# Kernel tuning notes

Measured on AMD Instinct MI355X. Metric: run time of the kernel, lower is better.

## Reference

```python
import jax, jax.numpy as jnp
import numpy as np

HIDDEN, HEADS, HDIM = 1024, 8, 64
B, S = 4, 8192
LN_EPS = 1e-6


def setup_inputs() -> dict:
    key = jax.random.key(0)
    ks = jax.random.split(key, 12)
    inner = HEADS * HDIM
    sd = HIDDEN ** -0.5
    return {
        "x": jax.random.normal(ks[0], (B, S, HIDDEN), jnp.float32),
        "Wq": jax.random.normal(ks[1], (HIDDEN, inner), jnp.float32) * sd,
        "bq": jnp.zeros((inner,), jnp.float32),
        "Wk": jax.random.normal(ks[2], (HIDDEN, inner), jnp.float32) * sd,
        "bk": jnp.zeros((inner,), jnp.float32),
        "Wv": jax.random.normal(ks[3], (HIDDEN, inner), jnp.float32) * sd,
        "bv": jnp.zeros((inner,), jnp.float32),
        "Wo": jax.random.normal(ks[4], (inner, HIDDEN), jnp.float32) * (inner ** -0.5),
        "bo": jnp.zeros((HIDDEN,), jnp.float32),
        "alpha": jnp.ones((HEADS, HDIM), jnp.float32),
        "aug_param": jax.random.normal(ks[5], (1, HEADS, HDIM), jnp.float32),
        "ln_scale": jnp.ones((HIDDEN,), jnp.float32),
        "ln_bias": jnp.zeros((HIDDEN,), jnp.float32),
    }


def reference(x, Wq, bq, Wk, bk, Wv, bv, Wo, bo, alpha, aug_param, ln_scale, ln_bias):
    b, s, _ = x.shape
    h, d = alpha.shape
    scale = d ** -0.5
    q = (x @ Wq + bq).reshape(b, s, h, d)
    k = (x @ Wk + bk).reshape(b, s, h, d)
    v = (x @ Wv + bv).reshape(b, s, h, d)
    decay = jax.nn.sigmoid(alpha)  # (h, d)

    def step(state, qkv):
        q_t, k_t, v_t = qkv  # each (b, h, d)
        attn = jax.nn.softmax(jnp.einsum('bhd,bhd->bh', q_t, k_t) * scale, axis=-1)
        new_state = decay * state + (1.0 - decay) * attn[..., None] * v_t
        return new_state, new_state

    qs = jnp.moveaxis(q, 1, 0)  # (s, b, h, d)
    ks_ = jnp.moveaxis(k, 1, 0)
    vs = jnp.moveaxis(v, 1, 0)
    init = jnp.zeros((b, h, d), x.dtype)
    _, states = jax.lax.scan(step, init, (qs, ks_, vs))
    states = jnp.moveaxis(states, 0, 1)  # (b, s, h, d)

    aug = jax.nn.sigmoid(q * aug_param)  # aug_param (1,h,d) broadcasts over (b,s,h,d)
    out = (q * states + aug).reshape(b, s, h * d)
    out = out @ Wo + bo
    mean = jnp.mean(out, axis=-1, keepdims=True)
    var = jnp.var(out, axis=-1, keepdims=True)
    return (out - mean) * jax.lax.rsqrt(var + LN_EPS) * ln_scale + ln_bias
```

## Files before the change

kernel.cpp:

```cpp
#include <hip/hip_runtime.h>
#include <hip/hip_bf16.h>


#define HIDDEN 1024
#define HEADS 8
#define HDIM 64
#define INNER 512
#define BATCH 4
#define SEQ 8192
#define ROWS (BATCH*SEQ)
#define NCHUNK 128
#define CHLEN 64

typedef unsigned short u16;
typedef unsigned int u32;
typedef __attribute__((ext_vector_type(8))) short bf16x8;
typedef __attribute__((ext_vector_type(4))) float f32x4;

__device__ __forceinline__ float b2f(u16 u) { return __uint_as_float(((u32)u) << 16); }
__device__ __forceinline__ u16 f2b(float f) {
  u32 u = __float_as_uint(f);
  u32 r = u + 0x7fffu + ((u >> 16) & 1u);
  return (u16)(r >> 16);
}
__device__ __forceinline__ u32 pack2(float a, float b) {
  return (u32)f2b(a) | ((u32)f2b(b) << 16);
}

#define GLOAD_LDS16(gp, lp)                                                  \
  __builtin_amdgcn_global_load_lds(                                          \
      (const __attribute__((address_space(1))) u32*)(gp),                    \
      (__attribute__((address_space(3))) u32*)(lp), 16, 0, 0)

__global__ __launch_bounds__(256) void prep_x(const float* __restrict__ x,
                                              u16* __restrict__ xb) {
  size_t i = ((size_t)blockIdx.x * 256 + threadIdx.x) * 8;
  float4 a = *(const float4*)(x + i);
  float4 b = *(const float4*)(x + i + 4);
  uint4 w = {pack2(a.x, a.y), pack2(a.z, a.w), pack2(b.x, b.y), pack2(b.z, b.w)};
  *(uint4*)(xb + i) = w;
}

__global__ __launch_bounds__(256) void prep_w(
    const float* __restrict__ Wq, const float* __restrict__ Wk,
    const float* __restrict__ Wv, const float* __restrict__ Wo,
    const float* __restrict__ bq, const float* __restrict__ bk,
    const float* __restrict__ bv,
    u16* __restrict__ Wt, u16* __restrict__ Wot, float* __restrict__ bcat) {
  const int WELEM = HIDDEN * INNER;
  int idx = blockIdx.x * 256 + threadIdx.x;
  if (idx < 3 * WELEM) {
    int z = idx / WELEM;
    int rem = idx - z * WELEM;
    int n = rem >> 10;
    int k = rem & 1023;
    const float* W = (z == 0) ? Wq : (z == 1) ? Wk : Wv;
    Wt[idx] = f2b(W[k * INNER + n]);
  } else {
    int rem = idx - 3 * WELEM;
    int n = rem >> 9;
    int k = rem & 511;
    Wot[rem] = f2b(Wo[k * HIDDEN + n]);
  }
  if (idx < 3 * INNER) {
    int z = idx >> 9;
    int n = idx & 511;
    bcat[idx] = (z == 0) ? bq[n] : (z == 1) ? bk[n] : bv[n];
  }
}

template <int K, bool SPLIT3>
__global__ __launch_bounds__(512, 2) void gemm_8ph(
    const u16* __restrict__ A, const u16* __restrict__ Bt,
    const float* __restrict__ bias,
    void* __restrict__ out0, void* __restrict__ out1, void* __restrict__ out2,
    int nTilesN) {
  constexpr int NT = K / 32;
  __shared__ u16 lds[4][16384];

  const int nwg = gridDim.x;
  const int chunk = nwg >> 3;
  const int bid = blockIdx.x;
  const int lin = (bid & 7) * chunk + (bid >> 3);
  const int nt = lin % nTilesN;
  const int mt = lin / nTilesN;
  const int m0 = mt * 256, n0 = nt * 256;
  const int N = nTilesN * 256;

  const int tid = threadIdx.x;
  const int lane = tid & 63;
  const int w = tid >> 6;
  const int wm = w >> 2;
  const int wn = w & 3;
  const int r16 = lane & 15, kq = lane >> 4;

  const int rt = tid >> 2;
  const int cg = (((tid & 3) << 3)) ^ (((rt >> 1) & 3) << 3);
  const u16* Ag = A + (size_t)(m0 + rt) * K + cg;
  const u16* Bg = Bt + (size_t)(n0 + rt) * K + cg;
  const int ldst = w * 512;

#define STAGE_AB(slot, kt)                                                    \
  {                                                                           \
    GLOAD_LDS16(Ag + (size_t)(kt) * 32, &lds[slot][ldst]);                    \
    GLOAD_LDS16(Ag + (size_t)(kt) * 32 + (size_t)128 * K,                     \
                &lds[slot][4096 + ldst]);                                     \
    GLOAD_LDS16(Bg + (size_t)(kt) * 32, &lds[slot][8192 + ldst]);             \
    GLOAD_LDS16(Bg + (size_t)(kt) * 32 + (size_t)128 * K,                     \
                &lds[slot][12288 + ldst]);                                    \
  }

  const int xk = (kq << 3) ^ (((r16 >> 1) & 3) << 3);
  const int aO = (wm * 128 + r16) * 32 + xk;
  const int bO = 8192 + (wn * 64 + r16) * 32 + xk;

  f32x4 acc[8][4] = {};

#define TILE(t_, STG, VMW)                                                     \
  {                                                                            \
    STG;                                                                       \
    const u16* sl = &lds[(t_) & 3][0];                                         \
    bf16x8 af0[4], af1[4], bfv4[4];                                            \
    _Pragma("unroll") for (int i = 0; i < 4; i++)                              \
        af0[i] = *(const bf16x8*)&sl[aO + i * 512];                            \
    _Pragma("unroll") for (int j = 0; j < 4; j++)                              \
        bfv4[j] = *(const bf16x8*)&sl[bO + j * 512];                           \
    __builtin_amdgcn_sched_barrier(0);                                         \
    _Pragma("unroll") for (int i = 0; i < 4; i++)                              \
        af1[i] = *(const bf16x8*)&sl[aO + (i + 4) * 512];                      \
    __builtin_amdgcn_sched_barrier(0);                                         \
    __builtin_amdgcn_s_setprio(1);                                             \
    _Pragma("unroll") for (int i = 0; i < 4; i++)                              \
        _Pragma("unroll") for (int j = 0; j < 4; j++)                          \
            acc[i][j] =                                                        \
        __builtin_amdgcn_mfma_f32_16x16x32_bf16(af0[i], bfv4[j], acc[i][j], 0, 0, 0); \
    __builtin_amdgcn_s_setprio(0);                                             \
    __builtin_amdgcn_sched_barrier(0);                                         \
    __builtin_amdgcn_s_setprio(1);                                             \
    _Pragma("unroll") for (int i = 0; i < 4; i++)                              \
        _Pragma("unroll") for (int j = 0; j < 4; j++)                          \
            acc[i + 4][j] =                                                    \
        __builtin_amdgcn_mfma_f32_16x16x32_bf16(af1[i], bfv4[j], acc[i + 4][j], 0, 0, 0); \
    __builtin_amdgcn_s_setprio(0);                                             \
    VMW;                                                                       \
    __builtin_amdgcn_sched_barrier(0);                                         \
    __builtin_amdgcn_s_barrier();                                              \
  }

#define VM8 asm volatile("s_waitcnt vmcnt(8)" ::: "memory")
#define VM4 asm volatile("s_waitcnt vmcnt(4)" ::: "memory")
#define VM0 asm volatile("s_waitcnt vmcnt(0)" ::: "memory")
#define NOSTG ((void)0)
#define NOVM ((void)0)

  STAGE_AB(0, 0);
  STAGE_AB(1, 1);
  STAGE_AB(2, 2);
  VM8;
  __builtin_amdgcn_sched_barrier(0);
  __builtin_amdgcn_s_barrier();

  for (int t = 0; t < NT - 3; ++t) {
    TILE(t, STAGE_AB((t + 3) & 3, t + 3), VM8);
  }
  TILE(NT - 3, NOSTG, VM4);
  TILE(NT - 2, NOSTG, VM0);
  TILE(NT - 1, NOSTG, NOVM);
#undef TILE
#undef STAGE_AB
#undef VM8
#undef VM4
#undef VM0
#undef NOSTG
#undef NOVM

  float* fl = (float*)(&lds[0][0]) + w * 4096;
  const int zsel = SPLIT3 ? ((n0 + wn * 64) >> 9) : 0;
  u16* ob = SPLIT3 ? (u16*)((zsel == 0) ? out0 : (zsel == 1) ? out1 : out2)
                   : (u16*)out0;
  const int OC = SPLIT3 ? INNER : N;
  const int colloc = (lane & 7) * 8;
  const int gcol = (SPLIT3 ? ((n0 + wn * 64) & 511) : (n0 + wn * 64)) + colloc;
  const int lrowr = lane >> 3;
  float bvj[4];
#pragma unroll
  for (int j = 0; j < 4; j++) bvj[j] = bias[n0 + wn * 64 + j * 16 + r16];

#pragma unroll
  for (int pass = 0; pass < 4; ++pass) {
#pragma unroll
    for (int ii = 0; ii < 2; ++ii) {
#pragma unroll
      for (int j = 0; j < 4; ++j) {
#pragma unroll
        for (int q = 0; q < 4; ++q)
          fl[(ii * 16 + kq * 4 + q) * 68 + j * 16 + r16] =
              acc[pass * 2 + ii][j][q] + bvj[j];
      }
    }
#pragma unroll
    for (int inst = 0; inst < 4; ++inst) {
      int lr = inst * 8 + lrowr;
      float4 f0 = *(float4*)&fl[lr * 68 + colloc];
      float4 f1 = *(float4*)&fl[lr * 68 + colloc + 4];
      uint4 wv = {pack2(f0.x, f0.y), pack2(f0.z, f0.w),
                  pack2(f1.x, f1.y), pack2(f1.z, f1.w)};
      size_t grow = (size_t)(m0 + wm * 128 + pass * 32 + lr);
      *(uint4*)&ob[grow * OC + gcol] = wv;
    }
  }
}

template <bool A_BF16>
__global__ __launch_bounds__(256) void gemm128(
    const void* __restrict__ Aany, const u16* __restrict__ BtBase,
    const float* __restrict__ bias0, const float* __restrict__ bias1,
    const float* __restrict__ bias2,
    void* __restrict__ out0, void* __restrict__ out1, void* __restrict__ out2,
    int K) {
  __shared__ u16 As[128 * 32];
  __shared__ u16 Bs[128 * 32];
  const int N = gridDim.x * 128;
  const int z = blockIdx.z;
  const u16* Bt = BtBase + (size_t)z * N * K;
  const float* bias = (z == 0) ? bias0 : (z == 1) ? bias1 : bias2;
  void* Out = (z == 0) ? out0 : (z == 1) ? out1 : out2;
  const int tid = threadIdx.x;
  const int m0 = blockIdx.y * 128;
  const int n0 = blockIdx.x * 128;
  const int lane = tid & 63;
  const int wid = tid >> 6;
  const int wm = wid >> 1, wn = wid & 1;
  const int r16 = lane & 15, kq = lane >> 4;
  const int r = tid >> 1;
  const int half = tid & 1;
  f32x4 acc[4][4] = {};
  for (int k0 = 0; k0 < K; k0 += 32) {
    __syncthreads();
    if (A_BF16) {
      const u16* Ab = (const u16*)Aany;
      const int4* src = (const int4*)(Ab + (size_t)(m0 + r) * K + k0 + half * 16);
      int4 v0 = src[0];
      int4 v1 = src[1];
      *(int4*)&As[r * 32 + half * 16] = v0;
      *(int4*)&As[r * 32 + half * 16 + 8] = v1;
    } else {
      const float* Af = (const float*)Aany;
      const float4* src = (const float4*)(Af + (size_t)(m0 + r) * K + k0 + half * 16);
      float4 f0 = src[0], f1 = src[1], f2 = src[2], f3 = src[3];
      uint4 w0 = {pack2(f0.x, f0.y), pack2(f0.z, f0.w), pack2(f1.x, f1.y), pack2(f1.z, f1.w)};
      uint4 w1 = {pack2(f2.x, f2.y), pack2(f2.z, f2.w), pack2(f3.x, f3.y), pack2(f3.z, f3.w)};
      *(uint4*)&As[r * 32 + half * 16] = w0;
      *(uint4*)&As[r * 32 + half * 16 + 8] = w1;
    }
    {
      const int4* src = (const int4*)(Bt + (size_t)(n0 + r) * K + k0 + half * 16);
      int4 v0 = src[0];
      int4 v1 = src[1];
      *(int4*)&Bs[r * 32 + half * 16] = v0;
      *(int4*)&Bs[r * 32 + half * 16 + 8] = v1;
    }
    __syncthreads();
    bf16x8 a[4], b[4];
#pragma unroll
    for (int i = 0; i < 4; i++)
      a[i] = *(const bf16x8*)&As[(wm * 64 + i * 16 + r16) * 32 + kq * 8];
#pragma unroll
    for (int j = 0; j < 4; j++)
      b[j] = *(const bf16x8*)&Bs[(wn * 64 + j * 16 + r16) * 32 + kq * 8];
#pragma unroll
    for (int i = 0; i < 4; i++)
#pragma unroll
      for (int j = 0; j < 4; j++)
        acc[i][j] = __builtin_amdgcn_mfma_f32_16x16x32_bf16(a[i], b[j], acc[i][j], 0, 0, 0);
  }
#pragma unroll
  for (int j = 0; j < 4; j++) {
    int col = n0 + wn * 64 + j * 16 + r16;
    float bv = bias[col];
#pragma unroll
    for (int i = 0; i < 4; i++) {
#pragma unroll
      for (int q = 0; q < 4; q++) {
        int row = m0 + wm * 64 + i * 16 + kq * 4 + q;
        float v = acc[i][j][q] + bv;
        ((u16*)Out)[(size_t)row * N + col] = f2b(v);
      }
    }
  }
}

__global__ __launch_bounds__(256) void attn_kernel(
    const u16* __restrict__ qb, const u16* __restrict__ kb,
    float* __restrict__ attn) {
  int lane = threadIdx.x & 63;
  int wid = threadIdx.x >> 6;
  size_t t = (size_t)blockIdx.x * 4 + wid;
  int4 qv = *(const int4*)(qb + t * INNER + lane * 8);
  int4 kv = *(const int4*)(kb + t * INNER + lane * 8);
  const u16* qu = (const u16*)&qv;
  const u16* ku = (const u16*)&kv;
  float s = 0.f;
#pragma unroll
  for (int j = 0; j < 8; j++) s += b2f(qu[j]) * b2f(ku[j]);
  s += __shfl_xor(s, 1);
  s += __shfl_xor(s, 2);
  s += __shfl_xor(s, 4);
  s *= 0.125f;
  float mx = s;
  mx = fmaxf(mx, __shfl_xor(mx, 8));
  mx = fmaxf(mx, __shfl_xor(mx, 16));
  mx = fmaxf(mx, __shfl_xor(mx, 32));
  float e = __expf(s - mx);
  float sm = e;
  sm += __shfl_xor(sm, 8);
  sm += __shfl_xor(sm, 16);
  sm += __shfl_xor(sm, 32);
  float a = e / sm;
  if ((lane & 7) == 0) attn[t * HEADS + (lane >> 3)] = a;
}

__global__ __launch_bounds__(512) void scan_phase1(
    const u16* __restrict__ vb, const float* __restrict__ attn,
    const float* __restrict__ alpha, float* __restrict__ ends) {
  int hd = threadIdx.x;
  int h = hd >> 6;
  int c = blockIdx.x, b = blockIdx.y;
  float decay = 1.f / (1.f + __expf(-alpha[hd]));
  float om = 1.f - decay;
  size_t base = (size_t)b * SEQ + (size_t)c * CHLEN;
  float st = 0.f;
#pragma unroll 8
  for (int i = 0; i < CHLEN; i++) {
    size_t t = base + i;
    float a = attn[t * HEADS + h];
    float v = b2f(vb[t * INNER + hd]);
    st = decay * st + om * a * v;
  }
  ends[((size_t)b * NCHUNK + c) * INNER + hd] = st;
}

__global__ __launch_bounds__(512) void scan_phase2(
    const float* __restrict__ ends, const float* __restrict__ alpha,
    float* __restrict__ carries) {
  int hd = threadIdx.x;
  int b = blockIdx.x;
  float decay = 1.f / (1.f + __expf(-alpha[hd]));
  float dL = __powf(decay, (float)CHLEN);
  float carry = 0.f;
#pragma unroll 8
  for (int c = 0; c < NCHUNK; c++) {
    size_t idx = ((size_t)b * NCHUNK + c) * INNER + hd;
    carries[idx] = carry;
    carry = dL * carry + ends[idx];
  }
}

__global__ __launch_bounds__(512) void scan_phase3(
    const u16* __restrict__ qb, const u16* __restrict__ vb,
    const float* __restrict__ attn, const float* __restrict__ alpha,
    const float* __restrict__ augp, const float* __restrict__ carries,
    u16* __restrict__ outpre) {
  int hd = threadIdx.x;
  int h = hd >> 6;
  int c = blockIdx.x, b = blockIdx.y;
  float decay = 1.f / (1.f + __expf(-alpha[hd]));
  float om = 1.f - decay;
  float ap = augp[hd];
  float st = carries[((size_t)b * NCHUNK + c) * INNER + hd];
  size_t base = (size_t)b * SEQ + (size_t)c * CHLEN;
#pragma unroll 4
  for (int i = 0; i < CHLEN; i++) {
    size_t t = base + i;
    float a = attn[t * HEADS + h];
    float v = b2f(vb[t * INNER + hd]);
    st = decay * st + om * a * v;
    float q = b2f(qb[t * INNER + hd]);
    float aug = 1.f / (1.f + __expf(-q * ap));
    outpre[t * INNER + hd] = f2b(q * st + aug);
  }
}

__global__ __launch_bounds__(256) void ln_kernel(
    const u16* __restrict__ outln, float* __restrict__ out,
    const float* __restrict__ lns, const float* __restrict__ lnb) {
  size_t row = blockIdx.x;
  int tid = threadIdx.x;
  uint2 rv = *(const uint2*)(outln + row * HIDDEN + tid * 4);
  const u16* p = (const u16*)&rv;
  float v0 = b2f(p[0]), v1 = b2f(p[1]), v2 = b2f(p[2]), v3 = b2f(p[3]);
  float s = v0 + v1 + v2 + v3;
  float ss = v0 * v0 + v1 * v1 + v2 * v2 + v3 * v3;
#pragma unroll
  for (int m = 1; m < 64; m <<= 1) {
    s += __shfl_xor(s, m);
    ss += __shfl_xor(ss, m);
  }
  __shared__ float sb[4], ssb[4];
  int lane = tid & 63, wid = tid >> 6;
  if (lane == 0) {
    sb[wid] = s;
    ssb[wid] = ss;
  }
  __syncthreads();
  s = sb[0] + sb[1] + sb[2] + sb[3];
  ss = ssb[0] + ssb[1] + ssb[2] + ssb[3];
  float mean = s * (1.f / HIDDEN);
  float var = ss * (1.f / HIDDEN) - mean * mean;
  float rstd = rsqrtf(var + 1e-6f);
  float4 sc = *(const float4*)(lns + tid * 4);
  float4 bi = *(const float4*)(lnb + tid * 4);
  float4 o;
  o.x = (v0 - mean) * rstd * sc.x + bi.x;
  o.y = (v1 - mean) * rstd * sc.y + bi.y;
  o.z = (v2 - mean) * rstd * sc.z + bi.z;
  o.w = (v3 - mean) * rstd * sc.w + bi.w;
  *(float4*)(out + row * HIDDEN + tid * 4) = o;
}

extern "C" void kernel_launch(void* const* d_in, const int* in_sizes, int n_in,
                              void* d_out, int out_size, void* d_ws, size_t ws_size,
                              hipStream_t stream) {
  const float* x = (const float*)d_in[0];
  const float* Wq = (const float*)d_in[1];
  const float* bq = (const float*)d_in[2];
  const float* Wk = (const float*)d_in[3];
  const float* bk = (const float*)d_in[4];
  const float* Wv = (const float*)d_in[5];
  const float* bv = (const float*)d_in[6];
  const float* Wo = (const float*)d_in[7];
  const float* bo = (const float*)d_in[8];
  const float* alpha = (const float*)d_in[9];
  const float* augp = (const float*)d_in[10];
  const float* lns = (const float*)d_in[11];
  const float* lnb = (const float*)d_in[12];

  char* ws = (char*)d_ws;
  const bool fast = ws_size >= 175118336ull;

  if (fast) {
    u16* xb = (u16*)(ws + 0);
    u16* qb = (u16*)(ws + 67108864);
    u16* kb = (u16*)(ws + 100663296);
    u16* vb = (u16*)(ws + 134217728);
    u16* Wt = (u16*)(ws + 167772160);
    u16* Wot = (u16*)(ws + 170917888);
    float* bcat = (float*)(ws + 171966464);
    float* attn = (float*)(ws + 171972608);
    float* ends = (float*)(ws + 173021184);
    float* car = (float*)(ws + 174069760);
    u16* outpre = kb;
    u16* outln = xb;

    prep_x<<<ROWS * HIDDEN / 8 / 256, 256, 0, stream>>>(x, xb);
    prep_w<<<8192, 256, 0, stream>>>(Wq, Wk, Wv, Wo, bq, bk, bv, Wt, Wot, bcat);

    gemm_8ph<HIDDEN, true><<<768, 512, 0, stream>>>(
        xb, Wt, bcat, qb, kb, vb, 6);

    attn_kernel<<<ROWS / 4, 256, 0, stream>>>(qb, kb, attn);
    scan_phase1<<<dim3(NCHUNK, BATCH), 512, 0, stream>>>(vb, attn, alpha, ends);
    scan_phase2<<<BATCH, 512, 0, stream>>>(ends, alpha, car);
    scan_phase3<<<dim3(NCHUNK, BATCH), 512, 0, stream>>>(qb, vb, attn, alpha, augp, car, outpre);

    gemm_8ph<INNER, false><<<512, 512, 0, stream>>>(
        outpre, Wot, bo, outln, outln, outln, 4);

    ln_kernel<<<ROWS, 256, 0, stream>>>(outln, (float*)d_out, lns, lnb);
  } else {
    u16* qb = (u16*)(ws + 0);
    u16* vb = (u16*)(ws + 33554432);
    u16* kb = (u16*)(ws + 67108864);
    u16* Wt = (u16*)(ws + 100663296);
    u16* Wot = (u16*)(ws + 103809024);
    float* bcat = (float*)(ws + 104845312);
    float* attn = (float*)(ws + 104857600);
    float* ends = (float*)(ws + 105906176);
    float* car = (float*)(ws + 106954752);
    u16* outpre = kb;
    u16* outln = (u16*)(ws + 0);

    prep_w<<<8192, 256, 0, stream>>>(Wq, Wk, Wv, Wo, bq, bk, bv, Wt, Wot, bcat);
    gemm128<false><<<dim3(4, 256, 3), 256, 0, stream>>>(
        x, Wt, bq, bk, bv, qb, kb, vb, HIDDEN);
    attn_kernel<<<ROWS / 4, 256, 0, stream>>>(qb, kb, attn);
    scan_phase1<<<dim3(NCHUNK, BATCH), 512, 0, stream>>>(vb, attn, alpha, ends);
    scan_phase2<<<BATCH, 512, 0, stream>>>(ends, alpha, car);
    scan_phase3<<<dim3(NCHUNK, BATCH), 512, 0, stream>>>(qb, vb, attn, alpha, augp, car, outpre);
    gemm_8ph<INNER, false><<<512, 512, 0, stream>>>(
        outpre, Wot, bo, outln, outln, outln, 4);
    ln_kernel<<<ROWS, 256, 0, stream>>>(outln, (float*)d_out, lns, lnb);
  }
}
```

Measured before the change: 275.1 us.

## Ping-pong register buffers to overlap LDS fragment reads with MFMA

Restructures the GEMM main loop, renaming the kernel to gemm_rp, so each K-tile's LDS fragments go into one of two register sets. The next tile's LDS reads are issued while the MFMAs on the current tile run. This is meant to hide LDS read latency behind matrix math and cuts the per-tile global-load wait from vmcnt(8) to vmcnt(4) with two tiles per loop iteration. In exchange it doubles the fragment registers held live, about 96 extra VGPRs next to 128 accumulator registers under a 512-thread, 2-block launch bound. That risks spills or lost occupancy.

New measurement: 273.6 us, median of 2. About the same (-0.5%).

```diff
diff --git a/kernel.cpp b/kernel.cpp
--- a/kernel.cpp
+++ b/kernel.cpp
@@ -70,7 +70,7 @@
 }
 
 template <int K, bool SPLIT3>
-__global__ __launch_bounds__(512, 2) void gemm_8ph(
+__global__ __launch_bounds__(512, 2) void gemm_rp(
     const u16* __restrict__ A, const u16* __restrict__ Bt,
     const float* __restrict__ bias,
     void* __restrict__ out0, void* __restrict__ out1, void* __restrict__ out2,
@@ -115,64 +115,75 @@
   const int bO = 8192 + (wn * 64 + r16) * 32 + xk;
 
   f32x4 acc[8][4] = {};
-
-#define TILE(t_, STG, VMW)                                                     \
+  bf16x8 r0_a[8], r0_b[4], r1_a[8], r1_b[4];
+
+#define DSREAD(da, db, slot)                                                   \
   {                                                                            \
-    STG;                                                                       \
-    const u16* sl = &lds[(t_) & 3][0];                                         \
-    bf16x8 af0[4], af1[4], bfv4[4];                                            \
-    _Pragma("unroll") for (int i = 0; i < 4; i++)                              \
-        af0[i] = *(const bf16x8*)&sl[aO + i * 512];                            \
+    const u16* sl = &lds[slot][0];                                             \
+    _Pragma("unroll") for (int i = 0; i < 8; i++)                              \
+        da[i] = *(const bf16x8*)&sl[aO + i * 512];                             \
     _Pragma("unroll") for (int j = 0; j < 4; j++)                              \
-        bfv4[j] = *(const bf16x8*)&sl[bO + j * 512];                           \
-    __builtin_amdgcn_sched_barrier(0);                                         \
-    _Pragma("unroll") for (int i = 0; i < 4; i++)                              \
-        af1[i] = *(const bf16x8*)&sl[aO + (i + 4) * 512];                      \
-    __builtin_amdgcn_sched_barrier(0);                                         \
+        db[j] = *(const bf16x8*)&sl[bO + j * 512];                             \
+  }
+
+#define MFMA_SET(sa, sb)                                                       \
+  {                                                                            \
     __builtin_amdgcn_s_setprio(1);                                             \
-    _Pragma("unroll") for (int i = 0; i < 4; i++)                              \
+    _Pragma("unroll") for (int i = 0; i < 8; i++)                              \
         _Pragma("unroll") for (int j = 0; j < 4; j++)                          \
-            acc[i][j] =                                                        \
-        __builtin_amdgcn_mfma_f32_16x16x32_bf16(af0[i], bfv4[j], acc[i][j], 0, 0, 0); \
+            acc[i][j] = __builtin_amdgcn_mfma_f32_16x16x32_bf16(               \
+                sa[i], sb[j], acc[i][j], 0, 0, 0);                             \
     __builtin_amdgcn_s_setprio(0);                                             \
-    __builtin_amdgcn_sched_barrier(0);                                         \
-    __builtin_amdgcn_s_setprio(1);                                             \
-    _Pragma("unroll") for (int i = 0; i < 4; i++)                              \
-        _Pragma("unroll") for (int j = 0; j < 4; j++)                          \
-            acc[i + 4][j] =                                                    \
-        __builtin_amdgcn_mfma_f32_16x16x32_bf16(af1[i], bfv4[j], acc[i + 4][j], 0, 0, 0); \
-    __builtin_amdgcn_s_setprio(0);                                             \
-    VMW;                                                                       \
+  }
+
+#define SYNCB                                                                  \
+  {                                                                            \
     __builtin_amdgcn_sched_barrier(0);                                         \
     __builtin_amdgcn_s_barrier();                                              \
-  }
-
-#define VM8 asm volatile("s_waitcnt vmcnt(8)" ::: "memory")
+    __builtin_amdgcn_sched_barrier(0);                                         \
+  }
+
 #define VM4 asm volatile("s_waitcnt vmcnt(4)" ::: "memory")
 #define VM0 asm volatile("s_waitcnt vmcnt(0)" ::: "memory")
-#define NOSTG ((void)0)
-#define NOVM ((void)0)
 
   STAGE_AB(0, 0);
   STAGE_AB(1, 1);
   STAGE_AB(2, 2);
-  VM8;
-  __builtin_amdgcn_sched_barrier(0);
-  __builtin_amdgcn_s_barrier();
-
-  for (int t = 0; t < NT - 3; ++t) {
-    TILE(t, STAGE_AB((t + 3) & 3, t + 3), VM8);
-  }
-  TILE(NT - 3, NOSTG, VM4);
-  TILE(NT - 2, NOSTG, VM0);
-  TILE(NT - 1, NOSTG, NOVM);
-#undef TILE
-#undef STAGE_AB
-#undef VM8
+  VM4;
+  SYNCB;
+  DSREAD(r0_a, r0_b, 0);
+
+  for (int t = 0; t + 6 <= NT; t += 2) {
+    STAGE_AB((t + 3) & 3, t + 3);
+    DSREAD(r1_a, r1_b, (t + 1) & 3);
+    MFMA_SET(r0_a, r0_b);
+    VM4;
+    SYNCB;
+    STAGE_AB((t + 4) & 3, t + 4);
+    DSREAD(r0_a, r0_b, (t + 2) & 3);
+    MFMA_SET(r1_a, r1_b);
+    VM4;
+    SYNCB;
+  }
+  STAGE_AB((NT - 1) & 3, NT - 1);
+  DSREAD(r1_a, r1_b, (NT - 3) & 3);
+  MFMA_SET(r0_a, r0_b);
+  VM4;
+  SYNCB;
+  DSREAD(r0_a, r0_b, (NT - 2) & 3);
+  MFMA_SET(r1_a, r1_b);
+  VM0;
+  SYNCB;
+  DSREAD(r1_a, r1_b, (NT - 1) & 3);
+  MFMA_SET(r0_a, r0_b);
+  MFMA_SET(r1_a, r1_b);
+  SYNCB;
+#undef DSREAD
+#undef MFMA_SET
+#undef SYNCB
 #undef VM4
 #undef VM0
-#undef NOSTG
-#undef NOVM
+#undef STAGE_AB
 
   float* fl = (float*)(&lds[0][0]) + w * 4096;
   const int zsel = SPLIT3 ? ((n0 + wn * 64) >> 9) : 0;
@@ -455,7 +466,7 @@
     prep_x<<<ROWS * HIDDEN / 8 / 256, 256, 0, stream>>>(x, xb);
     prep_w<<<8192, 256, 0, stream>>>(Wq, Wk, Wv, Wo, bq, bk, bv, Wt, Wot, bcat);
 
-    gemm_8ph<HIDDEN, true><<<768, 512, 0, stream>>>(
+    gemm_rp<HIDDEN, true><<<768, 512, 0, stream>>>(
         xb, Wt, bcat, qb, kb, vb, 6);
 
     attn_kernel<<<ROWS / 4, 256, 0, stream>>>(qb, kb, attn);
@@ -463,7 +474,7 @@
     scan_phase2<<<BATCH, 512, 0, stream>>>(ends, alpha, car);
     scan_phase3<<<dim3(NCHUNK, BATCH), 512, 0, stream>>>(qb, vb, attn, alpha, augp, car, outpre);
 
-    gemm_8ph<INNER, false><<<512, 512, 0, stream>>>(
+    gemm_rp<INNER, false><<<512, 512, 0, stream>>>(
         outpre, Wot, bo, outln, outln, outln, 4);
 
     ln_kernel<<<ROWS, 256, 0, stream>>>(outln, (float*)d_out, lns, lnb);
@@ -487,7 +498,7 @@
     scan_phase1<<<dim3(NCHUNK, BATCH), 512, 0, stream>>>(vb, attn, alpha, ends);
     scan_phase2<<<BATCH, 512, 0, stream>>>(ends, alpha, car);
     scan_phase3<<<dim3(NCHUNK, BATCH), 512, 0, stream>>>(qb, vb, attn, alpha, augp, car, outpre);
-    gemm_8ph<INNER, false><<<512, 512, 0, stream>>>(
+    gemm_rp<INNER, false><<<512, 512, 0, stream>>>(
         outpre, Wot, bo, outln, outln, outln, 4);
     ln_kernel<<<ROWS, 256, 0, stream>>>(outln, (float*)d_out, lns, lnb);
   }
```
